# Kernel optimization log

Measured on AMD Instinct MI355X. Metric: run time of the kernel, lower is better.

## Reference

```python
import jax, jax.numpy as jnp
import numpy as np

B, S, D_MODEL, N_HEADS = 2, 2048, 1024, 16
HEAD_DIM = D_MODEL // N_HEADS  # 64
SCALE = HEAD_DIM ** -0.5
MASK_FILL = -1e9


def setup_inputs() -> dict:
    key = jax.random.key(0)
    k1, k2, k3 = jax.random.split(key, 3)
    x = jax.random.normal(k1, (B, S, D_MODEL), dtype=jnp.float32)
    # nn.Linear weight [3*d_att, d_model], trunc_normal std=0.02 style init
    W_qkv = jax.random.normal(k2, (3 * D_MODEL, D_MODEL), dtype=jnp.float32) * 0.02
    # boolean attention mask over the full [b, s_q, h, t_k] score tensor (True = keep)
    mask = jax.random.bernoulli(k3, p=0.9, shape=(B, S, N_HEADS, S))
    return {"x": x, "W_qkv": W_qkv, "mask": mask}


def reference(x, W_qkv, mask):
    b, s, dm = x.shape
    h, d = N_HEADS, HEAD_DIM
    # fused QKV projection (no bias): [b,s,3*dm] -> [b,s,3,h,d]
    qkv = jnp.einsum('bsm,nm->bsn', x, W_qkv).reshape(b, s, 3, h, d)
    q, k, v = qkv[:, :, 0], qkv[:, :, 1], qkv[:, :, 2]
    # scores: [b, s_q, h, t_k]
    attn = jnp.einsum('bshd,bthd->bsht', q, k) * SCALE
    attn = jnp.where(mask, attn, MASK_FILL)
    attn = jax.nn.softmax(attn, axis=-1)
    # out[b,t,h,d] = sum_s attn[b,t,h,s] * v[b,s,h,d]  (original einsum 'b s h d, b t h s -> b t h d')
    out = jnp.einsum('bshd,bths->bthd', v, attn)
    return out.reshape(b, s, h * d)  # proj is Identity (d_out=None)
```

## Files before the change

kernel.cpp:

```cpp
#include <hip/hip_runtime.h>

#define S_   2048
#define DM_  1024
#define NH_  16
#define HD_  64
#define KDIM 1024
#define QB_  128

typedef __attribute__((ext_vector_type(8))) short  shortx8;
typedef __attribute__((ext_vector_type(4))) float  floatx4;

#define AS1 __attribute__((address_space(1)))
#define AS3 __attribute__((address_space(3)))

__device__ __forceinline__ unsigned short f2bf(float f) {
  unsigned u = __float_as_uint(f);
  u += 0x7FFFu + ((u >> 16) & 1u);
  return (unsigned short)(u >> 16);
}

__device__ __forceinline__ void gld_lds16(const void* g, unsigned short* l) {
  __builtin_amdgcn_global_load_lds((const AS1 void*)g, (AS3 void*)l, 16, 0, 0);
}

__global__ __launch_bounds__(256) void qkv_gemm(const void* __restrict__ Xv,
                                                const void* __restrict__ Wv,
                                                unsigned short* __restrict__ Qg,
                                                unsigned short* __restrict__ Kg,
                                                unsigned short* __restrict__ Vt)
{
  __shared__ unsigned short lA[128*64];
  __shared__ unsigned short lB[128*64];
  __shared__ int sx;
  const int tid  = threadIdx.x;
  const int wid  = tid >> 6,  lane = tid & 63;
  const int quad = lane >> 4, l16  = lane & 15;
  const int bm = blockIdx.x, bn = blockIdx.y;
  const int wM = (wid >> 1) * 64, wN = (wid & 1) * 64;

  if (tid == 0) sx = 0;
  __syncthreads();
  {
    unsigned xv = ((const unsigned*)Xv)[tid];
    unsigned b1 = (xv >> 8) & 0x7Fu;
    bool pb = (b1 >= 0x32u && b1 <= 0x41u);
    unsigned long long bal = __ballot(pb);
    if (lane == 0) atomicAdd(&sx, (int)__popcll(bal));
  }
  __syncthreads();
  const int xbf = sx > 128;

  floatx4 acc[4][4] = {};

  for (int kt = 0; kt < KDIM; kt += 64) {
    __syncthreads();
    if (xbf) {
      const unsigned short* X = (const unsigned short*)Xv;
      const unsigned short* W = (const unsigned short*)Wv;
      #pragma unroll
      for (int p = 0; p < 4; ++p) {
        int chunk = p*256 + tid;
        int r = chunk >> 3, c = chunk & 7;
        gld_lds16(X + (size_t)(bm*128 + r)*KDIM + kt + c*8, lA + chunk*8);
      }
      #pragma unroll
      for (int p = 0; p < 4; ++p) {
        int chunk = p*256 + tid;
        int r = chunk >> 3, c = chunk & 7;
        gld_lds16(W + (size_t)(bn*128 + r)*KDIM + kt + c*8, lB + chunk*8);
      }
    } else {
      const float* X = (const float*)Xv;
      const float* W = (const float*)Wv;
      #pragma unroll
      for (int p = 0; p < 8; ++p) {
        int c4 = p*256 + tid;
        int r = c4 >> 4, c = c4 & 15;
        float4 v = *(const float4*)(X + (size_t)(bm*128 + r)*KDIM + kt + c*4);
        unsigned short* d = lA + r*64 + c*4;
        d[0]=f2bf(v.x); d[1]=f2bf(v.y); d[2]=f2bf(v.z); d[3]=f2bf(v.w);
      }
      #pragma unroll
      for (int p = 0; p < 8; ++p) {
        int c4 = p*256 + tid;
        int r = c4 >> 4, c = c4 & 15;
        float4 v = *(const float4*)(W + (size_t)(bn*128 + r)*KDIM + kt + c*4);
        unsigned short* d = lB + r*64 + c*4;
        d[0]=f2bf(v.x); d[1]=f2bf(v.y); d[2]=f2bf(v.z); d[3]=f2bf(v.w);
      }
    }
    __syncthreads();

    #pragma unroll
    for (int ks = 0; ks < 2; ++ks) {
      shortx8 af[4], bfr[4];
      #pragma unroll
      for (int mi = 0; mi < 4; ++mi)
        af[mi] = *(const shortx8*)(lA + (wM + mi*16 + l16)*64 + ks*32 + quad*8);
      #pragma unroll
      for (int ni = 0; ni < 4; ++ni)
        bfr[ni] = *(const shortx8*)(lB + (wN + ni*16 + l16)*64 + ks*32 + quad*8);
      #pragma unroll
      for (int mi = 0; mi < 4; ++mi)
        #pragma unroll
        for (int ni = 0; ni < 4; ++ni)
          acc[mi][ni] = __builtin_amdgcn_mfma_f32_16x16x32_bf16(af[mi], bfr[ni], acc[mi][ni], 0, 0, 0);
    }
  }

  if (bn < 8) {
    #pragma unroll
    for (int mi = 0; mi < 4; ++mi)
      #pragma unroll
      for (int ni = 0; ni < 4; ++ni)
        #pragma unroll
        for (int r = 0; r < 4; ++r) {
          int m = bm*128 + wM + mi*16 + quad*4 + r;
          int n = bn*128 + wN + ni*16 + l16;
          int b = m >> 11, q = m & 2047, h = n >> 6, d = n & 63;
          Qg[(((size_t)(b*NH_ + h))*S_ + q)*HD_ + d] = f2bf(acc[mi][ni][r] * 0.125f);
        }
  } else if (bn < 16) {
    #pragma unroll
    for (int mi = 0; mi < 4; ++mi)
      #pragma unroll
      for (int ni = 0; ni < 4; ++ni)
        #pragma unroll
        for (int r = 0; r < 4; ++r) {
          int m = bm*128 + wM + mi*16 + quad*4 + r;
          int n = bn*128 + wN + ni*16 + l16 - 1024;
          int b = m >> 11, t = m & 2047, h = n >> 6, d = n & 63;
          Kg[(((size_t)(b*NH_ + h))*S_ + t)*HD_ + d] = f2bf(acc[mi][ni][r]);
        }
  } else {
    #pragma unroll
    for (int mi = 0; mi < 4; ++mi)
      #pragma unroll
      for (int ni = 0; ni < 4; ++ni) {
        int m0 = bm*128 + wM + mi*16 + quad*4;
        int n  = bn*128 + wN + ni*16 + l16 - 2048;
        int b = m0 >> 11, t = m0 & 2047, h = n >> 6, d = n & 63;
        ushort4 u;
        u.x = f2bf(acc[mi][ni][0]); u.y = f2bf(acc[mi][ni][1]);
        u.z = f2bf(acc[mi][ni][2]); u.w = f2bf(acc[mi][ni][3]);
        *(ushort4*)(Vt + (((size_t)(b*NH_ + h))*HD_ + d)*S_ + t) = u;
      }
  }
}

__global__ __launch_bounds__(256, 2) void attn_kernel(const unsigned short* __restrict__ Qg,
                                                      const unsigned short* __restrict__ Kg,
                                                      const unsigned short* __restrict__ Vt,
                                                      const void* __restrict__ maskp,
                                                      const void* __restrict__ xg,
                                                      void* __restrict__ outv)
{
  __shared__ unsigned short lQ[QB_*HD_];
  __shared__ unsigned short lK[2][64*HD_];
  __shared__ unsigned short lVt[2][HD_*64];
  __shared__ int sdet[5];

  const int tid  = threadIdx.x;
  const int wid  = tid >> 6,  lane = tid & 63;
  const int quad = lane >> 4, l16  = lane & 15;
  const int qb = blockIdx.x * QB_;
  const int h  = blockIdx.y, b = blockIdx.z;
  const int bh = b*NH_ + h;

  if (tid < 5) sdet[tid] = (tid == 4) ? 0 : 1;
  __syncthreads();
  {
    unsigned mv = ((const unsigned*)maskp)[tid];
    bool o32  = (mv <= 1u);
    bool of32 = (mv == 0u) || (mv == 0x3F800000u);
    unsigned lo = mv & 0xFFFFu, hi = mv >> 16;
    bool o16 = ((lo==0u)||(lo==0x3F80u)) && ((hi==0u)||(hi==0x3F80u));
    bool o8  = ((mv & 0xFEFEFEFEu) == 0u);
    unsigned xv = ((const unsigned*)xg)[tid];
    unsigned b1 = (xv >> 8) & 0x7Fu;
    bool pb = (b1 >= 0x32u && b1 <= 0x41u);
    unsigned long long B0 = __ballot(o32), B1 = __ballot(of32);
    unsigned long long B2 = __ballot(o16), B3 = __ballot(o8);
    unsigned long long BX = __ballot(pb);
    if (lane == 0) {
      if (~B0) atomicAnd(&sdet[0], 0);
      if (~B1) atomicAnd(&sdet[1], 0);
      if (~B2) atomicAnd(&sdet[2], 0);
      if (~B3) atomicAnd(&sdet[3], 0);
      atomicAdd(&sdet[4], (int)__popcll(BX));
    }
  }

  #pragma unroll
  for (int p = 0; p < 4; ++p) {
    int chunk = p*256 + tid;
    gld_lds16(Qg + ((size_t)bh*S_ + qb)*HD_ + chunk*8, lQ + chunk*8);
  }

  auto stage = [&](int t0, int buf) {
    #pragma unroll
    for (int p = 0; p < 2; ++p) {
      int chunk = p*256 + tid;
      gld_lds16(Kg + ((size_t)bh*S_ + t0)*HD_ + chunk*8, lK[buf] + chunk*8);
    }
    #pragma unroll
    for (int p = 0; p < 2; ++p) {
      int chunk = p*256 + tid;
      int r = chunk >> 3, c = chunk & 7;
      gld_lds16(Vt + ((size_t)bh*HD_ + r)*S_ + t0 + c*8, lVt[buf] + chunk*8);
    }
  };

  size_t mrow[2][4];
  #pragma unroll
  for (int qh = 0; qh < 2; ++qh)
    #pragma unroll
    for (int r = 0; r < 4; ++r) {
      int q = qb + wid*32 + qh*16 + quad*4 + r;
      mrow[qh][r] = (((size_t)b*S_ + q)*NH_ + h)*S_ + l16;
    }

  stage(0, 0);
  __syncthreads();

  const int mflag = sdet[0] ? 0 : (sdet[1] ? 3 : (sdet[2] ? 2 : 1));
  const int obf   = sdet[4] > 128;

  auto loadraw = [&](int t0, unsigned (*mz)[4][4]) {
    if (mflag == 1) {
      const unsigned char* mp = (const unsigned char*)maskp;
      #pragma unroll
      for (int qh = 0; qh < 2; ++qh)
        #pragma unroll
        for (int r = 0; r < 4; ++r)
          #pragma unroll
          for (int tile = 0; tile < 4; ++tile) mz[qh][r][tile] = mp[mrow[qh][r] + t0 + tile*16];
    } else if (mflag == 2) {
      const unsigned short* mp = (const unsigned short*)maskp;
      #pragma unroll
      for (int qh = 0; qh < 2; ++qh)
        #pragma unroll
        for (int r = 0; r < 4; ++r)
          #pragma unroll
          for (int tile = 0; tile < 4; ++tile) mz[qh][r][tile] = mp[mrow[qh][r] + t0 + tile*16];
    } else {
      const unsigned* mp = (const unsigned*)maskp;
      #pragma unroll
      for (int qh = 0; qh < 2; ++qh)
        #pragma unroll
        for (int r = 0; r < 4; ++r)
          #pragma unroll
          for (int tile = 0; tile < 4; ++tile) mz[qh][r][tile] = mp[mrow[qh][r] + t0 + tile*16];
    }
  };

  shortx8 qf[2][2];
  #pragma unroll
  for (int qh = 0; qh < 2; ++qh)
    #pragma unroll
    for (int ks = 0; ks < 2; ++ks)
      qf[qh][ks] = *(const shortx8*)(lQ + (wid*32 + qh*16 + l16)*HD_ + ks*32 + quad*8);

  floatx4 acc[2][4] = {};
  float lsum[2][4] = {};
  unsigned short* lPw = lQ + wid*2048;

  unsigned mc = 0;
  {
    unsigned m0[2][4][4];
    loadraw(0, m0);
    #pragma unroll
    for (int qh = 0; qh < 2; ++qh)
      #pragma unroll
      for (int r = 0; r < 4; ++r)
        #pragma unroll
        for (int tile = 0; tile < 4; ++tile)
          mc |= (m0[qh][r][tile] != 0u ? 1u : 0u) << (qh*16 + r*4 + tile);
  }

  for (int t0 = 0; t0 < S_; t0 += 64) {
    const int cur = (t0 >> 6) & 1;
    unsigned mraw[2][4][4];
    const bool more = (t0 + 64 < S_);
    if (more) {
      stage(t0 + 64, cur ^ 1);
      loadraw(t0 + 64, mraw);
    }

    #pragma unroll
    for (int qh = 0; qh < 2; ++qh) {
      floatx4 sc[4] = {};
      #pragma unroll
      for (int tile = 0; tile < 4; ++tile)
        #pragma unroll
        for (int ks = 0; ks < 2; ++ks) {
          shortx8 kf = *(const shortx8*)(lK[cur] + (tile*16 + l16)*64 + ks*32 + quad*8);
          sc[tile] = __builtin_amdgcn_mfma_f32_16x16x32_bf16(qf[qh][ks], kf, sc[tile], 0, 0, 0);
        }

      #pragma unroll
      for (int tile = 0; tile < 4; ++tile)
        #pragma unroll
        for (int r = 0; r < 4; ++r) {
          float e = __expf(sc[tile][r]);
          e = (mc & (1u << (qh*16 + r*4 + tile))) ? e : 0.f;
          lsum[qh][r] += e;
          int row = qh*16 + quad*4 + r;
          int col = tile*16 + l16;
          lPw[(row << 6) + (((col >> 3) ^ (row & 7)) << 3) + (col & 7)] = f2bf(e);
        }

      #pragma unroll
      for (int ks = 0; ks < 2; ++ks) {
        int prow = qh*16 + l16;
        shortx8 pa = *(const shortx8*)(lPw + (prow << 6) + (((ks*4 + quad) ^ (prow & 7)) << 3));
        #pragma unroll
        for (int d = 0; d < 4; ++d) {
          shortx8 vb = *(const shortx8*)(lVt[cur] + (d*16 + l16)*64 + ks*32 + quad*8);
          acc[qh][d] = __builtin_amdgcn_mfma_f32_16x16x32_bf16(pa, vb, acc[qh][d], 0, 0, 0);
        }
      }
    }

    unsigned mcn = 0;
    if (more) {
      #pragma unroll
      for (int qh = 0; qh < 2; ++qh)
        #pragma unroll
        for (int r = 0; r < 4; ++r)
          #pragma unroll
          for (int tile = 0; tile < 4; ++tile)
            mcn |= (mraw[qh][r][tile] != 0u ? 1u : 0u) << (qh*16 + r*4 + tile);
    }
    __syncthreads();
    mc = mcn;
  }

  float rinv[2][4];
  #pragma unroll
  for (int qh = 0; qh < 2; ++qh)
    #pragma unroll
    for (int r = 0; r < 4; ++r) {
      float l = lsum[qh][r];
      #pragma unroll
      for (int o = 1; o < 16; o <<= 1) l += __shfl_xor(l, o);
      rinv[qh][r] = 1.f / l;
    }

  #pragma unroll
  for (int qh = 0; qh < 2; ++qh)
    #pragma unroll
    for (int d = 0; d < 4; ++d)
      #pragma unroll
      for (int r = 0; r < 4; ++r) {
        int q = qb + wid*32 + qh*16 + quad*4 + r;
        size_t oi = ((size_t)b*S_ + q)*DM_ + h*HD_ + d*16 + l16;
        float v = acc[qh][d][r] * rinv[qh][r];
        if (obf) ((unsigned short*)outv)[oi] = f2bf(v);
        else     ((float*)outv)[oi]          = v;
      }
}

extern "C" void kernel_launch(void* const* d_in, const int* in_sizes, int n_in,
                              void* d_out, int out_size, void* d_ws, size_t ws_size,
                              hipStream_t stream) {
  (void)in_sizes; (void)n_in; (void)out_size; (void)ws_size;
  const void* X    = d_in[0];
  const void* W    = d_in[1];
  const void* mask = d_in[2];
  const size_t SEG = (size_t)2*NH_*S_*HD_*2;
  unsigned short* Qg = (unsigned short*)((char*)d_ws + 256);
  unsigned short* Kg = (unsigned short*)((char*)d_ws + 256 + SEG);
  unsigned short* Vt = (unsigned short*)((char*)d_ws + 256 + 2*SEG);

  qkv_gemm<<<dim3(32, 24), 256, 0, stream>>>(X, W, Qg, Kg, Vt);
  attn_kernel<<<dim3(S_/QB_, NH_, 2), 256, 0, stream>>>(Qg, Kg, Vt, mask, X, d_out);
}
```

Before: 851.1 us.

## Pre-pack attention mask into bitmasks inside QKV GEMM launch, read bits in attention

Extra blocks in the QKV GEMM grid convert the boolean mask into 64-bit ballot words stored in workspace. The attention kernel then loads one word per row per 64-key tile instead of many scattered byte loads, removing per-element mask gathers from the inner loop. The attention inner loop is also reorganised so both query halves share each K/V fragment load for MFMA. This adds a full pass over the mask plus a packed-mask write, and relies on the workspace holding that extra buffer.

```diff
diff --git a/kernel.cpp b/kernel.cpp
--- a/kernel.cpp
+++ b/kernel.cpp
@@ -6,6 +6,7 @@
 #define HD_  64
 #define KDIM 1024
 #define QB_  128
+#define NWORDS (2u*S_*NH_*S_/64u)
 
 typedef __attribute__((ext_vector_type(8))) short  shortx8;
 typedef __attribute__((ext_vector_type(4))) float  floatx4;
@@ -23,19 +24,76 @@
   __builtin_amdgcn_global_load_lds((const AS1 void*)g, (AS3 void*)l, 16, 0, 0);
 }
 
-__global__ __launch_bounds__(256) void qkv_gemm(const void* __restrict__ Xv,
-                                                const void* __restrict__ Wv,
-                                                unsigned short* __restrict__ Qg,
-                                                unsigned short* __restrict__ Kg,
-                                                unsigned short* __restrict__ Vt)
+__global__ __launch_bounds__(256) void qkv_gemm_pack(const void* __restrict__ Xv,
+                                                     const void* __restrict__ Wv,
+                                                     const void* __restrict__ maskp,
+                                                     unsigned short* __restrict__ Qg,
+                                                     unsigned short* __restrict__ Kg,
+                                                     unsigned short* __restrict__ Vt,
+                                                     unsigned long long* __restrict__ pk)
 {
+  const int tid  = threadIdx.x;
+  const int wid  = tid >> 6,  lane = tid & 63;
+
+  if (blockIdx.y < 8) {
+    __shared__ int psd[3];
+    if (tid < 3) psd[tid] = 1;
+    __syncthreads();
+    {
+      unsigned mv = ((const unsigned*)maskp)[tid];
+      bool w4 = (mv <= 1u) || (mv == 0x3F800000u);
+      unsigned lo = mv & 0xFFFFu, hi = mv >> 16;
+      bool w2 = ((lo==0u)||(lo==0x3F80u)) && ((hi==0u)||(hi==0x3F80u));
+      unsigned long long B4 = __ballot(w4), B2 = __ballot(w2);
+      if (lane == 0) {
+        if (~B4) atomicAnd(&psd[0], 0);
+        if (~B2) atomicAnd(&psd[1], 0);
+      }
+    }
+    __syncthreads();
+    const int esz = psd[0] ? 4 : (psd[1] ? 2 : 1);
+
+    const int pid = blockIdx.y * 32 + blockIdx.x;
+    const unsigned gw = (unsigned)(pid*4 + wid);
+    unsigned wbase = gw * (NWORDS/1024u);
+    for (int rnd = 0; rnd < (int)(NWORDS/1024u/16u); ++rnd) {
+      unsigned w0 = wbase + rnd*16;
+      unsigned long long B[16];
+      if (esz == 4) {
+        const unsigned* mp = (const unsigned*)maskp;
+        unsigned v[16];
+        #pragma unroll
+        for (int j = 0; j < 16; ++j) v[j] = mp[(size_t)(w0+j)*64 + lane];
+        #pragma unroll
+        for (int j = 0; j < 16; ++j) B[j] = __ballot(v[j] != 0u);
+      } else if (esz == 2) {
+        const unsigned short* mp = (const unsigned short*)maskp;
+        unsigned short v[16];
+        #pragma unroll
+        for (int j = 0; j < 16; ++j) v[j] = mp[(size_t)(w0+j)*64 + lane];
+        #pragma unroll
+        for (int j = 0; j < 16; ++j) B[j] = __ballot(v[j] != 0);
+      } else {
+        const unsigned char* mp = (const unsigned char*)maskp;
+        unsigned char v[16];
+        #pragma unroll
+        for (int j = 0; j < 16; ++j) v[j] = mp[(size_t)(w0+j)*64 + lane];
+        #pragma unroll
+        for (int j = 0; j < 16; ++j) B[j] = __ballot(v[j] != 0);
+      }
+      if (lane == 0) {
+        #pragma unroll
+        for (int j = 0; j < 16; ++j) pk[w0 + j] = B[j];
+      }
+    }
+    return;
+  }
+
   __shared__ unsigned short lA[128*64];
   __shared__ unsigned short lB[128*64];
   __shared__ int sx;
-  const int tid  = threadIdx.x;
-  const int wid  = tid >> 6,  lane = tid & 63;
   const int quad = lane >> 4, l16  = lane & 15;
-  const int bm = blockIdx.x, bn = blockIdx.y;
+  const int bm = blockIdx.x, bn = blockIdx.y - 8;
   const int wM = (wid >> 1) * 64, wN = (wid & 1) * 64;
 
   if (tid == 0) sx = 0;
@@ -151,14 +209,14 @@
 __global__ __launch_bounds__(256, 2) void attn_kernel(const unsigned short* __restrict__ Qg,
                                                       const unsigned short* __restrict__ Kg,
                                                       const unsigned short* __restrict__ Vt,
-                                                      const void* __restrict__ maskp,
+                                                      const unsigned long long* __restrict__ pk,
                                                       const void* __restrict__ xg,
                                                       void* __restrict__ outv)
 {
   __shared__ unsigned short lQ[QB_*HD_];
   __shared__ unsigned short lK[2][64*HD_];
   __shared__ unsigned short lVt[2][HD_*64];
-  __shared__ int sdet[5];
+  __shared__ int sdet;
 
   const int tid  = threadIdx.x;
   const int wid  = tid >> 6,  lane = tid & 63;
@@ -167,28 +225,14 @@
   const int h  = blockIdx.y, b = blockIdx.z;
   const int bh = b*NH_ + h;
 
-  if (tid < 5) sdet[tid] = (tid == 4) ? 0 : 1;
+  if (tid == 0) sdet = 0;
   __syncthreads();
   {
-    unsigned mv = ((const unsigned*)maskp)[tid];
-    bool o32  = (mv <= 1u);
-    bool of32 = (mv == 0u) || (mv == 0x3F800000u);
-    unsigned lo = mv & 0xFFFFu, hi = mv >> 16;
-    bool o16 = ((lo==0u)||(lo==0x3F80u)) && ((hi==0u)||(hi==0x3F80u));
-    bool o8  = ((mv & 0xFEFEFEFEu) == 0u);
     unsigned xv = ((const unsigned*)xg)[tid];
     unsigned b1 = (xv >> 8) & 0x7Fu;
     bool pb = (b1 >= 0x32u && b1 <= 0x41u);
-    unsigned long long B0 = __ballot(o32), B1 = __ballot(of32);
-    unsigned long long B2 = __ballot(o16), B3 = __ballot(o8);
     unsigned long long BX = __ballot(pb);
-    if (lane == 0) {
-      if (~B0) atomicAnd(&sdet[0], 0);
-      if (~B1) atomicAnd(&sdet[1], 0);
-      if (~B2) atomicAnd(&sdet[2], 0);
-      if (~B3) atomicAnd(&sdet[3], 0);
-      atomicAdd(&sdet[4], (int)__popcll(BX));
-    }
+    if (lane == 0) atomicAdd(&sdet, (int)__popcll(BX));
   }
 
   #pragma unroll
@@ -211,48 +255,22 @@
     }
   };
 
-  size_t mrow[2][4];
-  #pragma unroll
-  for (int qh = 0; qh < 2; ++qh)
-    #pragma unroll
-    for (int r = 0; r < 4; ++r) {
-      int q = qb + wid*32 + qh*16 + quad*4 + r;
-      mrow[qh][r] = (((size_t)b*S_ + q)*NH_ + h)*S_ + l16;
-    }
-
+  const size_t mw0 = ((size_t)(b*S_ + qb + wid*32 + quad*4)*NH_ + h)*(S_/64);
+
+  auto loadw = [&](int t0, unsigned long long* w) {
+    int wi = t0 >> 6;
+    #pragma unroll
+    for (int qh = 0; qh < 2; ++qh)
+      #pragma unroll
+      for (int r = 0; r < 4; ++r)
+        w[qh*4+r] = pk[mw0 + (size_t)(qh*16 + r)*512 + wi];
+  };
+
+  unsigned long long wc[8], wn[8];
   stage(0, 0);
+  loadw(0, wc);
   __syncthreads();
-
-  const int mflag = sdet[0] ? 0 : (sdet[1] ? 3 : (sdet[2] ? 2 : 1));
-  const int obf   = sdet[4] > 128;
-
-  auto loadraw = [&](int t0, unsigned (*mz)[4][4]) {
-    if (mflag == 1) {
-      const unsigned char* mp = (const unsigned char*)maskp;
-      #pragma unroll
-      for (int qh = 0; qh < 2; ++qh)
-        #pragma unroll
-        for (int r = 0; r < 4; ++r)
-          #pragma unroll
-          for (int tile = 0; tile < 4; ++tile) mz[qh][r][tile] = mp[mrow[qh][r] + t0 + tile*16];
-    } else if (mflag == 2) {
-      const unsigned short* mp = (const unsigned short*)maskp;
-      #pragma unroll
-      for (int qh = 0; qh < 2; ++qh)
-        #pragma unroll
-        for (int r = 0; r < 4; ++r)
-          #pragma unroll
-          for (int tile = 0; tile < 4; ++tile) mz[qh][r][tile] = mp[mrow[qh][r] + t0 + tile*16];
-    } else {
-      const unsigned* mp = (const unsigned*)maskp;
-      #pragma unroll
-      for (int qh = 0; qh < 2; ++qh)
-        #pragma unroll
-        for (int r = 0; r < 4; ++r)
-          #pragma unroll
-          for (int tile = 0; tile < 4; ++tile) mz[qh][r][tile] = mp[mrow[qh][r] + t0 + tile*16];
-    }
-  };
+  const int obf = sdet > 128;
 
   shortx8 qf[2][2];
   #pragma unroll
@@ -265,75 +283,60 @@
   float lsum[2][4] = {};
   unsigned short* lPw = lQ + wid*2048;
 
-  unsigned mc = 0;
-  {
-    unsigned m0[2][4][4];
-    loadraw(0, m0);
-    #pragma unroll
-    for (int qh = 0; qh < 2; ++qh)
-      #pragma unroll
-      for (int r = 0; r < 4; ++r)
-        #pragma unroll
-        for (int tile = 0; tile < 4; ++tile)
-          mc |= (m0[qh][r][tile] != 0u ? 1u : 0u) << (qh*16 + r*4 + tile);
-  }
-
   for (int t0 = 0; t0 < S_; t0 += 64) {
     const int cur = (t0 >> 6) & 1;
-    unsigned mraw[2][4][4];
     const bool more = (t0 + 64 < S_);
     if (more) {
       stage(t0 + 64, cur ^ 1);
-      loadraw(t0 + 64, mraw);
-    }
-
-    #pragma unroll
-    for (int qh = 0; qh < 2; ++qh) {
-      floatx4 sc[4] = {};
-      #pragma unroll
-      for (int tile = 0; tile < 4; ++tile)
-        #pragma unroll
-        for (int ks = 0; ks < 2; ++ks) {
-          shortx8 kf = *(const shortx8*)(lK[cur] + (tile*16 + l16)*64 + ks*32 + quad*8);
-          sc[tile] = __builtin_amdgcn_mfma_f32_16x16x32_bf16(qf[qh][ks], kf, sc[tile], 0, 0, 0);
-        }
-
-      #pragma unroll
-      for (int tile = 0; tile < 4; ++tile)
-        #pragma unroll
-        for (int r = 0; r < 4; ++r) {
-          float e = __expf(sc[tile][r]);
-          e = (mc & (1u << (qh*16 + r*4 + tile))) ? e : 0.f;
+      loadw(t0 + 64, wn);
+    }
+
+    floatx4 sc[2][4] = {};
+    #pragma unroll
+    for (int tile = 0; tile < 4; ++tile)
+      #pragma unroll
+      for (int ks = 0; ks < 2; ++ks) {
+        shortx8 kf = *(const shortx8*)(lK[cur] + (tile*16 + l16)*64 + ks*32 + quad*8);
+        sc[0][tile] = __builtin_amdgcn_mfma_f32_16x16x32_bf16(qf[0][ks], kf, sc[0][tile], 0, 0, 0);
+        sc[1][tile] = __builtin_amdgcn_mfma_f32_16x16x32_bf16(qf[1][ks], kf, sc[1][tile], 0, 0, 0);
+      }
+
+    #pragma unroll
+    for (int qh = 0; qh < 2; ++qh)
+      #pragma unroll
+      for (int r = 0; r < 4; ++r) {
+        unsigned long long w = wc[qh*4+r] >> l16;
+        #pragma unroll
+        for (int tile = 0; tile < 4; ++tile) {
+          float e = __expf(sc[qh][tile][r]);
+          e = ((w >> (tile*16)) & 1ull) ? e : 0.f;
           lsum[qh][r] += e;
           int row = qh*16 + quad*4 + r;
           int col = tile*16 + l16;
           lPw[(row << 6) + (((col >> 3) ^ (row & 7)) << 3) + (col & 7)] = f2bf(e);
         }
-
+      }
+
+    shortx8 pa[2][2];
+    #pragma unroll
+    for (int qh = 0; qh < 2; ++qh)
       #pragma unroll
       for (int ks = 0; ks < 2; ++ks) {
         int prow = qh*16 + l16;
-        shortx8 pa = *(const shortx8*)(lPw + (prow << 6) + (((ks*4 + quad) ^ (prow & 7)) << 3));
-        #pragma unroll
-        for (int d = 0; d < 4; ++d) {
-          shortx8 vb = *(const shortx8*)(lVt[cur] + (d*16 + l16)*64 + ks*32 + quad*8);
-          acc[qh][d] = __builtin_amdgcn_mfma_f32_16x16x32_bf16(pa, vb, acc[qh][d], 0, 0, 0);
-        }
-      }
-    }
-
-    unsigned mcn = 0;
-    if (more) {
-      #pragma unroll
-      for (int qh = 0; qh < 2; ++qh)
-        #pragma unroll
-        for (int r = 0; r < 4; ++r)
-          #pragma unroll
-          for (int tile = 0; tile < 4; ++tile)
-            mcn |= (mraw[qh][r][tile] != 0u ? 1u : 0u) << (qh*16 + r*4 + tile);
-    }
-    __syncthreads();
-    mc = mcn;
+        pa[qh][ks] = *(const shortx8*)(lPw + (prow << 6) + (((ks*4 + quad) ^ (prow & 7)) << 3));
+      }
+    #pragma unroll
+    for (int ks = 0; ks < 2; ++ks)
+      #pragma unroll
+      for (int d = 0; d < 4; ++d) {
+        shortx8 vb = *(const shortx8*)(lVt[cur] + (d*16 + l16)*64 + ks*32 + quad*8);
+        acc[0][d] = __builtin_amdgcn_mfma_f32_16x16x32_bf16(pa[0][ks], vb, acc[0][d], 0, 0, 0);
+        acc[1][d] = __builtin_amdgcn_mfma_f32_16x16x32_bf16(pa[1][ks], vb, acc[1][d], 0, 0, 0);
+      }
+
+    #pragma unroll
+    for (int i = 0; i < 8; ++i) wc[i] = wn[i];
+    __syncthreads();
   }
 
   float rinv[2][4];
@@ -372,7 +375,8 @@
   unsigned short* Qg = (unsigned short*)((char*)d_ws + 256);
   unsigned short* Kg = (unsigned short*)((char*)d_ws + 256 + SEG);
   unsigned short* Vt = (unsigned short*)((char*)d_ws + 256 + 2*SEG);
-
-  qkv_gemm<<<dim3(32, 24), 256, 0, stream>>>(X, W, Qg, Kg, Vt);
-  attn_kernel<<<dim3(S_/QB_, NH_, 2), 256, 0, stream>>>(Qg, Kg, Vt, mask, X, d_out);
-}
+  unsigned long long* pk = (unsigned long long*)((char*)d_ws + 256 + 3*SEG);
+
+  qkv_gemm_pack<<<dim3(32, 32), 256, 0, stream>>>(X, W, mask, Qg, Kg, Vt, pk);
+  attn_kernel<<<dim3(S_/QB_, NH_, 2), 256, 0, stream>>>(Qg, Kg, Vt, pk, X, d_out);
+}
```

Measured after the change: 890.5 us. 1.05x slower.
